# Kernel tuning notes

Hardware: AMD Instinct MI355X
Metric: run time of the kernel (lower is better)

Reference implementation:

```python
import jax, jax.numpy as jnp
import numpy as np

N_NODES = 50000
N_EDGES = 600000
N_GRAPHS = 512
HID = 128
LAT = 64
L = 4
BN_EPS = 1e-5


def _gelu(x):
    return jax.nn.gelu(x, approximate=False)


def _bn(x, g, b):
    m = jnp.mean(x, axis=0)
    v = jnp.var(x, axis=0)
    return (x - m) * jax.lax.rsqrt(v + BN_EPS) * g + b


def setup_inputs() -> dict:
    key = jax.random.key(0)
    ks = jax.random.split(key, 8)
    x = jax.random.normal(ks[0], (N_NODES, HID), dtype=jnp.float32)
    edge_index = jax.random.randint(ks[1], (2, N_EDGES), 0, N_NODES, dtype=jnp.int64 if jax.config.jax_enable_x64 else jnp.int32)
    batch = jnp.sort(jax.random.randint(ks[2], (N_NODES,), 0, N_GRAPHS))
    scale = 1.0 / np.sqrt(HID)
    return {
        "x": x,
        "edge_index": edge_index,
        "batch": batch,
        "input_bn_g": jnp.ones((HID,), jnp.float32),
        "input_bn_b": jnp.zeros((HID,), jnp.float32),
        "eps": jnp.zeros((L,), jnp.float32),
        "fc1_w": jax.random.normal(ks[3], (L, HID, HID), jnp.float32) * scale,
        "fc1_b": jnp.zeros((L, HID), jnp.float32),
        "bn1_g": jnp.ones((L, HID), jnp.float32),
        "bn1_b": jnp.zeros((L, HID), jnp.float32),
        "fc2_w": jax.random.normal(ks[4], (L, HID, HID), jnp.float32) * scale,
        "fc2_b": jnp.zeros((L, HID), jnp.float32),
        "bn_g": jnp.ones((L, HID), jnp.float32),
        "bn_b": jnp.zeros((L, HID), jnp.float32),
        "att_weight": jax.random.normal(ks[5], (L, HID), jnp.float32),
        "pool_weight": jnp.ones((3,), jnp.float32),
        "fcA_w": jax.random.normal(ks[6], (HID, HID), jnp.float32) * scale,
        "fcA_b": jnp.zeros((HID,), jnp.float32),
        "ln_g": jnp.ones((HID,), jnp.float32),
        "ln_b": jnp.zeros((HID,), jnp.float32),
        "fcB_w": jax.random.normal(ks[7], (HID, LAT), jnp.float32) * scale,
        "fcB_b": jnp.zeros((LAT,), jnp.float32),
    }


def reference(x, edge_index, batch, input_bn_g, input_bn_b, eps, fc1_w, fc1_b,
              bn1_g, bn1_b, fc2_w, fc2_b, bn_g, bn_b, att_weight, pool_weight,
              fcA_w, fcA_b, ln_g, ln_b, fcB_w, fcB_b):
    src, dst = edge_index[0], edge_index[1]
    x = _bn(x, input_bn_g, input_bn_b)  # input BatchNorm (batch stats)
    hidden_states = []
    for l in range(L):
        # GINConv: (1+eps)*x_i + sum_{j->i} x_j, then GatedResidualMLP
        agg = jax.ops.segment_sum(x[src], dst, num_segments=N_NODES)
        h = (1.0 + eps[l]) * x + agg
        h = _gelu(_bn(h @ fc1_w[l] + fc1_b[l], bn1_g[l], bn1_b[l]))
        h = h @ fc2_w[l] + fc2_b[l]
        h = _gelu(_bn(h, bn_g[l], bn_b[l]))
        hidden_states.append(h)
        x = h
    # JumpingKnowledge attention over layers
    x_all = jnp.stack(hidden_states, axis=0)               # [L, N, H]
    scores = jnp.mean(x_all * att_weight[:, None, :], -1)  # [L, N]
    alpha = jax.nn.softmax(scores, axis=0)
    x = jnp.sum(x_all * alpha[..., None], axis=0)          # [N, H]
    # fused add/mean/max pooling by graph id
    pw = jax.nn.softmax(pool_weight)
    sums = jax.ops.segment_sum(x, batch, num_segments=N_GRAPHS)
    cnt = jax.ops.segment_sum(jnp.ones((N_NODES, 1), x.dtype), batch, num_segments=N_GRAPHS)
    mean = sums / jnp.maximum(cnt, 1.0)
    mx = jax.ops.segment_max(x, batch, num_segments=N_GRAPHS)
    mx = jnp.where(cnt > 0, mx, 0.0)
    pooled = sums * pw[0] + mean * pw[1] + mx * pw[2]      # [G, H]
    out = pooled @ fcA_w + fcA_b
    mu = jnp.mean(out, -1, keepdims=True)
    var = jnp.var(out, -1, keepdims=True)
    out = (out - mu) * jax.lax.rsqrt(var + 1e-5) * ln_g + ln_b
    out = _gelu(out) + pooled
    return out @ fcB_w + fcB_b                              # [G, latent]
```

## Files before the change

kernel.cpp:

```cpp
#include <hip/hip_runtime.h>
#include <math.h>

#define N_NODES 50000
#define N_EDGES 600000
#define N_GRAPHS 512
#define HID 128
#define LAT 64
#define NL 4
#define SSTR 16
#define SSET 4096
#define N_TILES 3125
#define ZROWS 208
#define ZLD 136

typedef __attribute__((ext_vector_type(8))) __bf16 bf16x8;
typedef __attribute__((ext_vector_type(4))) float f32x4;

union Chunk {
    bf16x8 v;
    uint4 u4;
    ushort us[8];
};

__device__ __forceinline__ float gelu_exact(float x) {
    return 0.5f * x * (1.0f + erff(x * 0.70710678118654752f));
}
__device__ __forceinline__ float gelu_fast(float x) {
    float ax = fabsf(x) * 0.70710678118654752f;
    float t = __builtin_amdgcn_rcpf(fmaf(0.3275911f, ax, 1.0f));
    float p = t * (0.254829592f +
              t * (-0.284496736f +
              t * (1.421413741f +
              t * (-1.453152027f + t * 1.061405429f))));
    float e = __expf(-ax * ax);
    float erfv = 1.0f - p * e;
    float erfs = copysignf(erfv, x);
    return 0.5f * x * (1.0f + erfs);
}
__device__ __forceinline__ float bf2f(ushort h) {
    return __uint_as_float(((unsigned int)h) << 16);
}
__device__ __forceinline__ ushort f2bf(float f) {
    unsigned int u = __float_as_uint(f);
    unsigned int r = (u + 0x7FFFu + ((u >> 16) & 1u)) >> 16;
    return (ushort)r;
}
__device__ __forceinline__ void atomicMaxF(float* addr, float v) {
    if (v >= 0.f) atomicMax((int*)addr, __float_as_int(v));
    else atomicMin((unsigned int*)addr, __float_as_uint(v));
}

__device__ __forceinline__ void sub_range(int p, int j, int& s0, int& s1) {
    int r0 = (p * N_NODES) >> 8;
    int r1 = ((p + 1) * N_NODES) >> 8;
    int len = r1 - r0;
    s0 = r0 + ((len * j) >> 3);
    s1 = r0 + ((len * (j + 1)) >> 3);
}

template <bool NEWBAR>
__device__ __forceinline__ void grid_sync(int* bar, int epoch) {
    __syncthreads();
    if (threadIdx.x == 0) {
        int target = 256 * epoch;
        int prev = __hip_atomic_fetch_add(bar, 1, __ATOMIC_RELAXED,
                                          __HIP_MEMORY_SCOPE_AGENT);
        if (NEWBAR) {
            if (prev == target - 1) {
                __hip_atomic_store(bar + 32, epoch, __ATOMIC_RELAXED,
                                   __HIP_MEMORY_SCOPE_AGENT);
            } else {
                while (__hip_atomic_load(bar + 32, __ATOMIC_RELAXED,
                                         __HIP_MEMORY_SCOPE_AGENT) < epoch)
                    __builtin_amdgcn_s_sleep(8);
            }
        } else {
            while (__hip_atomic_load(bar, __ATOMIC_RELAXED,
                                     __HIP_MEMORY_SCOPE_AGENT) < target)
                __builtin_amdgcn_s_sleep(2);
        }
    }
    __syncthreads();
    asm volatile("" ::: "memory");
}

__device__ __forceinline__ float coh_ld(const float* p) {
    return __hip_atomic_load((const float*)p, __ATOMIC_RELAXED, __HIP_MEMORY_SCOPE_AGENT);
}

__global__ __launch_bounds__(256) void setup(const float* __restrict__ fc1w,
                                             const float* __restrict__ fc2w,
                                             ushort* __restrict__ Wt,
                                             int* __restrict__ counts,
                                             float* __restrict__ statsAll,
                                             float* __restrict__ psum,
                                             float* __restrict__ pmax,
                                             int* __restrict__ gstart,
                                             int* __restrict__ gend,
                                             int* __restrict__ bar) {
    int i = blockIdx.x * 256 + threadIdx.x;
    {
        int g = i >> 14;
        int rem = i & 16383;
        int n = rem >> 7, k = rem & 127;
        const float* W = (g < 4) ? (fc1w + (long)g * HID * HID)
                                 : (fc2w + (long)(g - 4) * HID * HID);
        Wt[i] = f2bf(W[k * HID + n]);
    }
    if (i < N_NODES) counts[i] = 0;
    if (i < 9 * SSET) statsAll[i] = 0.f;
    if (i < N_GRAPHS * HID) { psum[i] = 0.f; pmax[i] = -INFINITY; }
    if (i < N_GRAPHS) { gstart[i] = 0; gend[i] = 0; }
    if (i < 64) bar[i] = 0;
}

__global__ __launch_bounds__(256) void stats_count(const float* __restrict__ X,
                                                   float* __restrict__ stats,
                                                   const int* __restrict__ dst,
                                                   int* __restrict__ counts,
                                                   const int* __restrict__ batch,
                                                   int* __restrict__ gstart,
                                                   int* __restrict__ gend) {
    __shared__ float sh[2048];
    int bx = blockIdx.x;
    int t = threadIdx.x;
    if (bx < 256) {
        int tx = t & 31, ty = t >> 5;
        float s[4] = {0, 0, 0, 0}, q[4] = {0, 0, 0, 0};
        const int nTiles = (N_NODES + 63) / 64;
        for (int tile = bx; tile < nTiles; tile += 256) {
            int r0 = tile * 64;
#pragma unroll
            for (int i = 0; i < 8; ++i) {
                int r = r0 + ty + 8 * i;
                int rc = min(r, N_NODES - 1);
                float4 v = *(const float4*)(X + (long)rc * HID + 4 * tx);
                float w = (r < N_NODES) ? 1.f : 0.f;
                float x0 = v.x * w, x1 = v.y * w, x2 = v.z * w, x3 = v.w * w;
                s[0] += x0; s[1] += x1; s[2] += x2; s[3] += x3;
                q[0] += x0 * v.x; q[1] += x1 * v.y; q[2] += x2 * v.z; q[3] += x3 * v.w;
            }
        }
#pragma unroll
        for (int c = 0; c < 4; ++c) {
            sh[ty * HID + 4 * tx + c] = s[c];
            sh[1024 + ty * HID + 4 * tx + c] = q[c];
        }
        __syncthreads();
        if (ty == 0) {
#pragma unroll
            for (int c = 0; c < 4; ++c) {
                float a = 0, b = 0;
#pragma unroll
                for (int j = 0; j < 8; ++j) {
                    a += sh[j * HID + 4 * tx + c];
                    b += sh[1024 + j * HID + 4 * tx + c];
                }
                atomicAdd(stats + (4 * tx + c) * SSTR, a);
                atomicAdd(stats + (HID + 4 * tx + c) * SSTR, b);
            }
        }
    } else if (bx < 2600) {
        int e = (bx - 256) * 256 + t;
        if (e < N_EDGES) atomicAdd(counts + dst[e], 1);
    } else {
        int n = (bx - 2600) * 256 + t;
        if (n < N_NODES) {
            int b = batch[n];
            if (n == 0 || batch[n - 1] != b) gstart[b] = n;
            if (n == N_NODES - 1 || batch[n + 1] != b) gend[b] = n + 1;
        }
    }
}

__global__ __launch_bounds__(256) void bn_scan(const float* __restrict__ X,
                                               ushort* __restrict__ Y,
                                               const float* __restrict__ stats,
                                               const float* __restrict__ g,
                                               const float* __restrict__ b,
                                               const int* __restrict__ counts,
                                               int* __restrict__ offs,
                                               int* __restrict__ bsum) {
    __shared__ float scL[HID], sfL[HID];
    __shared__ int shI[256];
    int t = threadIdx.x;
    if (t < HID) {
        const float invN = 1.0f / (float)N_NODES;
        float mean = stats[t * SSTR] * invN;
        float var = stats[(HID + t) * SSTR] * invN - mean * mean;
        float s = g[t] * rsqrtf(var + 1e-5f);
        scL[t] = s;
        sfL[t] = b[t] - mean * s;
    }
    __syncthreads();
    int c4 = (t & 31) * 4;
    float sc[4], sf[4];
#pragma unroll
    for (int j = 0; j < 4; ++j) { sc[j] = scL[c4 + j]; sf[j] = sfL[c4 + j]; }
    int s0, s1;
    sub_range(blockIdx.x & 255, blockIdx.x >> 8, s0, s1);
    int c0 = s0 * 32, c1 = s1 * 32;
    for (int i = c0 + t; i < c1; i += 256) {
        float4 v = ((const float4*)X)[i];
        ushort4 w;
        w.x = f2bf(v.x * sc[0] + sf[0]);
        w.y = f2bf(v.y * sc[1] + sf[1]);
        w.z = f2bf(v.z * sc[2] + sf[2]);
        w.w = f2bf(v.w * sc[3] + sf[3]);
        ((ushort4*)Y)[i] = w;
    }
    if (blockIdx.x < 196) {
        int i = blockIdx.x * 256 + t;
        int v = (i < N_NODES) ? counts[i] : 0;
        shI[t] = v;
        __syncthreads();
        for (int off = 1; off < 256; off <<= 1) {
            int a = (t >= off) ? shI[t - off] : 0;
            __syncthreads();
            shI[t] += a;
            __syncthreads();
        }
        if (i < N_NODES) offs[i] = shI[t] - v;
        if (t == 255) bsum[blockIdx.x] = shI[255];
    }
}

__global__ __launch_bounds__(256) void scan23(int* __restrict__ offs,
                                              const int* __restrict__ bsum,
                                              int* __restrict__ cursor) {
    __shared__ int sh[256];
    int t = threadIdx.x, bx = blockIdx.x;
    int v = (t < bx) ? bsum[t] : 0;
    sh[t] = v;
    __syncthreads();
    for (int off = 128; off > 0; off >>= 1) {
        if (t < off) sh[t] += sh[t + off];
        __syncthreads();
    }
    int pre = sh[0];
    int i = bx * 256 + t;
    if (i < N_NODES) {
        int o = offs[i] + pre;
        offs[i] = o;
        cursor[i] = o;
    }
}

__global__ __launch_bounds__(256) void csr_fill(const int* __restrict__ src,
                                                const int* __restrict__ dst,
                                                int* __restrict__ cursor,
                                                int* __restrict__ csr) {
    int e = blockIdx.x * blockDim.x + threadIdx.x;
    if (e >= N_EDGES) return;
    int pos = atomicAdd(cursor + dst[e], 1);
    csr[pos] = src[e];
}

__global__ __launch_bounds__(256) void gin_gather_bf(const ushort* __restrict__ Xbf,
                                                     ushort* __restrict__ Hp,
                                                     const int* __restrict__ offs,
                                                     const int* __restrict__ counts,
                                                     const int* __restrict__ csr,
                                                     const float* __restrict__ eps, int l) {
    int t = threadIdx.x;
    int tx = t & 31;
    int grp = t >> 5;
    int s0, s1;
    sub_range(blockIdx.x & 255, blockIdx.x >> 8, s0, s1);
    float ev = 1.0f + eps[l];
    for (int node = s0 + grp; node < s1; node += 8) {
        ushort4 sv = *(const ushort4*)(Xbf + (long)node * HID + 4 * tx);
        float a0 = bf2f(sv.x) * ev, a1 = bf2f(sv.y) * ev;
        float a2 = bf2f(sv.z) * ev, a3 = bf2f(sv.w) * ev;
        int o = offs[node];
        int d = counts[node];
        int k = 0;
        for (; k + 8 <= d; k += 8) {
            int si[8];
#pragma unroll
            for (int j = 0; j < 8; ++j) si[j] = csr[o + k + j];
            ushort4 v[8];
#pragma unroll
            for (int j = 0; j < 8; ++j)
                v[j] = *(const ushort4*)(Xbf + (long)si[j] * HID + 4 * tx);
#pragma unroll
            for (int j = 0; j < 8; ++j) {
                a0 += bf2f(v[j].x); a1 += bf2f(v[j].y);
                a2 += bf2f(v[j].z); a3 += bf2f(v[j].w);
            }
        }
        for (; k + 4 <= d; k += 4) {
            int si[4];
#pragma unroll
            for (int j = 0; j < 4; ++j) si[j] = csr[o + k + j];
#pragma unroll
            for (int j = 0; j < 4; ++j) {
                ushort4 v = *(const ushort4*)(Xbf + (long)si[j] * HID + 4 * tx);
                a0 += bf2f(v.x); a1 += bf2f(v.y); a2 += bf2f(v.z); a3 += bf2f(v.w);
            }
        }
        for (; k < d; ++k) {
            int s = csr[o + k];
            ushort4 v = *(const ushort4*)(Xbf + (long)s * HID + 4 * tx);
            a0 += bf2f(v.x); a1 += bf2f(v.y); a2 += bf2f(v.z); a3 += bf2f(v.w);
        }
        ushort4 w;
        w.x = f2bf(a0); w.y = f2bf(a1); w.z = f2bf(a2); w.w = f2bf(a3);
        *(ushort4*)(Hp + (long)node * HID + 4 * tx) = w;
    }
}

template <int NT, bool NEWBAR>
__global__ __launch_bounds__(NT, 1) void fused_mlp(
    const ushort* __restrict__ Abf, const ushort* __restrict__ W1t,
    const ushort* __restrict__ W2t, const float* __restrict__ b1v,
    const float* __restrict__ b2v, const float* __restrict__ bn1g,
    const float* __restrict__ bn1b, const float* __restrict__ bn2g,
    const float* __restrict__ bn2b, float* __restrict__ st1,
    float* __restrict__ st2, ushort* __restrict__ Hl, int* __restrict__ bar,
    int epoch0) {
    constexpr int NW = NT / 64;
    constexpr int RSTEP = NW / 2;
    __shared__ __align__(16) ushort Z1[ZROWS * ZLD];
    __shared__ __align__(16) ushort Z2[ZROWS * ZLD];
    __shared__ float shs[2 * NT];
    __shared__ float scL[HID], sfL[HID];

    int t = threadIdx.x;
    int w = t >> 6, lane = t & 63;
    int m = lane & 15, q = lane >> 4;
    int c2 = w & 1, r2 = w >> 1;
    int t0 = (blockIdx.x * N_TILES) >> 8;
    int t1 = ((blockIdx.x + 1) * N_TILES) >> 8;

    bf16x8 Bf[4][4];
    {
        const ushort* Wh = W1t + (long)(c2 * 64) * HID;
#pragma unroll
        for (int nt = 0; nt < 4; ++nt)
#pragma unroll
            for (int kc = 0; kc < 4; ++kc)
                Bf[nt][kc] = *(const bf16x8*)(Wh + (nt * 16 + m) * HID + kc * 32 + q * 8);
    }
    float bias4[4];
#pragma unroll
    for (int nt = 0; nt < 4; ++nt) bias4[nt] = b1v[c2 * 64 + nt * 16 + m];

    float s_c[4] = {0, 0, 0, 0}, q_c[4] = {0, 0, 0, 0};
    int tile = t0 + r2;
    Chunk Ac[4];
    if (tile < t1) {
        const ushort* ar = Abf + (long)(tile * 16 + m) * HID + q * 8;
#pragma unroll
        for (int kc = 0; kc < 4; ++kc) Ac[kc].u4 = *(const uint4*)(ar + kc * 32);
    }
    while (tile < t1) {
        int nxt = tile + RSTEP;
        Chunk An[4];
        if (nxt < t1) {
            const ushort* ar = Abf + (long)(nxt * 16 + m) * HID + q * 8;
#pragma unroll
            for (int kc = 0; kc < 4; ++kc) An[kc].u4 = *(const uint4*)(ar + kc * 32);
        }
        f32x4 acc[4];
#pragma unroll
        for (int nt = 0; nt < 4; ++nt) acc[nt] = (f32x4){0.f, 0.f, 0.f, 0.f};
#pragma unroll
        for (int kc = 0; kc < 4; ++kc)
#pragma unroll
            for (int nt = 0; nt < 4; ++nt)
                acc[nt] = __builtin_amdgcn_mfma_f32_16x16x32_bf16(Ac[kc].v, Bf[nt][kc],
                                                                  acc[nt], 0, 0, 0);
        int lrow = (tile - t0) * 16;
#pragma unroll
        for (int nt = 0; nt < 4; ++nt) {
            int col = c2 * 64 + nt * 16 + m;
#pragma unroll
            for (int r = 0; r < 4; ++r) {
                float z = acc[nt][r] + bias4[nt];
                Z1[(lrow + q * 4 + r) * ZLD + col] = f2bf(z);
                s_c[nt] += z;
                q_c[nt] += z * z;
            }
        }
        tile = nxt;
#pragma unroll
        for (int kc = 0; kc < 4; ++kc) Ac[kc] = An[kc];
    }
#pragma unroll
    for (int nt = 0; nt < 4; ++nt) {
        s_c[nt] += __shfl_xor(s_c[nt], 16);
        s_c[nt] += __shfl_xor(s_c[nt], 32);
        q_c[nt] += __shfl_xor(q_c[nt], 16);
        q_c[nt] += __shfl_xor(q_c[nt], 32);
    }
    if (q == 0) {
#pragma unroll
        for (int nt = 0; nt < 4; ++nt) {
            shs[w * 64 + nt * 16 + m] = s_c[nt];
            shs[NT + w * 64 + nt * 16 + m] = q_c[nt];
        }
    }
    __syncthreads();
    if (t < HID) {
        int half = t >> 6, lc = t & 63;
        float a = 0.f, b = 0.f;
#pragma unroll
        for (int j = 0; j < RSTEP; ++j) {
            a += shs[(half + 2 * j) * 64 + lc];
            b += shs[NT + (half + 2 * j) * 64 + lc];
        }
        atomicAdd(st1 + t * SSTR, a);
        atomicAdd(st1 + (HID + t) * SSTR, b);
    }
    grid_sync<NEWBAR>(bar, epoch0 + 1);

    if (t < HID) {
        const float invN = 1.0f / (float)N_NODES;
        float mean = coh_ld(st1 + t * SSTR) * invN;
        float var = coh_ld(st1 + (HID + t) * SSTR) * invN - mean * mean;
        float s = bn1g[t] * rsqrtf(var + 1e-5f);
        scL[t] = s;
        sfL[t] = bn1b[t] - mean * s;
    }
    __syncthreads();

    {
        const ushort* Wh = W2t + (long)(c2 * 64) * HID;
#pragma unroll
        for (int nt = 0; nt < 4; ++nt)
#pragma unroll
            for (int kc = 0; kc < 4; ++kc)
                Bf[nt][kc] = *(const bf16x8*)(Wh + (nt * 16 + m) * HID + kc * 32 + q * 8);
    }
#pragma unroll
    for (int nt = 0; nt < 4; ++nt) bias4[nt] = b2v[c2 * 64 + nt * 16 + m];
#pragma unroll
    for (int nt = 0; nt < 4; ++nt) { s_c[nt] = 0.f; q_c[nt] = 0.f; }

    for (int tl = t0 + r2; tl < t1; tl += RSTEP) {
        int lrow = (tl - t0) * 16;
        Chunk Ax[4];
#pragma unroll
        for (int kc = 0; kc < 4; ++kc)
            Ax[kc].u4 = *(const uint4*)(Z1 + (lrow + m) * ZLD + kc * 32 + q * 8);
#pragma unroll
        for (int kc = 0; kc < 4; ++kc)
#pragma unroll
            for (int j = 0; j < 8; ++j) {
                int k = kc * 32 + q * 8 + j;
                float f = bf2f(Ax[kc].us[j]) * scL[k] + sfL[k];
                Ax[kc].us[j] = f2bf(gelu_fast(f));
            }
        f32x4 acc[4];
#pragma unroll
        for (int nt = 0; nt < 4; ++nt) acc[nt] = (f32x4){0.f, 0.f, 0.f, 0.f};
#pragma unroll
        for (int kc = 0; kc < 4; ++kc)
#pragma unroll
            for (int nt = 0; nt < 4; ++nt)
                acc[nt] = __builtin_amdgcn_mfma_f32_16x16x32_bf16(Ax[kc].v, Bf[nt][kc],
                                                                  acc[nt], 0, 0, 0);
#pragma unroll
        for (int nt = 0; nt < 4; ++nt) {
            int col = c2 * 64 + nt * 16 + m;
#pragma unroll
            for (int r = 0; r < 4; ++r) {
                float z = acc[nt][r] + bias4[nt];
                Z2[(lrow + q * 4 + r) * ZLD + col] = f2bf(z);
                s_c[nt] += z;
                q_c[nt] += z * z;
            }
        }
    }
#pragma unroll
    for (int nt = 0; nt < 4; ++nt) {
        s_c[nt] += __shfl_xor(s_c[nt], 16);
        s_c[nt] += __shfl_xor(s_c[nt], 32);
        q_c[nt] += __shfl_xor(q_c[nt], 16);
        q_c[nt] += __shfl_xor(q_c[nt], 32);
    }
    if (q == 0) {
#pragma unroll
        for (int nt = 0; nt < 4; ++nt) {
            shs[w * 64 + nt * 16 + m] = s_c[nt];
            shs[NT + w * 64 + nt * 16 + m] = q_c[nt];
        }
    }
    __syncthreads();
    if (t < HID) {
        int half = t >> 6, lc = t & 63;
        float a = 0.f, b = 0.f;
#pragma unroll
        for (int j = 0; j < RSTEP; ++j) {
            a += shs[(half + 2 * j) * 64 + lc];
            b += shs[NT + (half + 2 * j) * 64 + lc];
        }
        atomicAdd(st2 + t * SSTR, a);
        atomicAdd(st2 + (HID + t) * SSTR, b);
    }
    grid_sync<NEWBAR>(bar, epoch0 + 2);

    if (t < HID) {
        const float invN = 1.0f / (float)N_NODES;
        float mean = coh_ld(st2 + t * SSTR) * invN;
        float var = coh_ld(st2 + (HID + t) * SSTR) * invN - mean * mean;
        float s = bn2g[t] * rsqrtf(var + 1e-5f);
        scL[t] = s;
        sfL[t] = bn2b[t] - mean * s;
    }
    __syncthreads();

    int nch = (t1 - t0) * 16 * 16;
    for (int i = t; i < nch; i += NT) {
        int row = i >> 4, off = i & 15;
        Chunk ch;
        ch.u4 = *(const uint4*)(Z2 + row * ZLD + off * 8);
#pragma unroll
        for (int j = 0; j < 8; ++j) {
            int cc = off * 8 + j;
            float f = bf2f(ch.us[j]) * scL[cc] + sfL[cc];
            ch.us[j] = f2bf(gelu_fast(f));
        }
        *(uint4*)(Hl + (long)(t0 * 16 + row) * HID + off * 8) = ch.u4;
    }
}

__global__ __launch_bounds__(256) void jk_pool(const ushort* __restrict__ H0,
                                               const ushort* __restrict__ H1,
                                               const ushort* __restrict__ H2,
                                               const ushort* __restrict__ H3,
                                               const float* __restrict__ att,
                                               const int* __restrict__ batch,
                                               float* __restrict__ psum,
                                               float* __restrict__ pmax) {
    int t = threadIdx.x;
    int lane = t & 63, w = t >> 6;
    long wid = (long)blockIdx.x * 4 + w;
    int a0 = (int)((wid * N_NODES) >> 13);
    int a1 = (int)(((wid + 1) * N_NODES) >> 13);
    const ushort* Hs[4] = {H0, H1, H2, H3};
    float2 av[4];
#pragma unroll
    for (int l = 0; l < 4; ++l) av[l] = *(const float2*)(att + l * HID + 2 * lane);

    int curg = -1;
    float sx = 0.f, sy = 0.f, mx = -INFINITY, my = -INFINITY;
    for (int node = a0; node < a1; ++node) {
        int g = batch[node];
        if (g != curg) {
            if (curg >= 0) {
                float* ps = psum + (long)curg * HID + 2 * lane;
                float* pm = pmax + (long)curg * HID + 2 * lane;
                atomicAdd(ps, sx);
                atomicAdd(ps + 1, sy);
                atomicMaxF(pm, mx);
                atomicMaxF(pm + 1, my);
            }
            curg = g;
            sx = 0.f; sy = 0.f; mx = -INFINITY; my = -INFINITY;
        }
        float hx[4], hy[4], scr[4];
#pragma unroll
        for (int l = 0; l < 4; ++l) {
            unsigned int u = *(const unsigned int*)(Hs[l] + (long)node * HID + 2 * lane);
            float vx = bf2f((ushort)(u & 0xFFFF));
            float vy = bf2f((ushort)(u >> 16));
            hx[l] = vx; hy[l] = vy;
            float p = vx * av[l].x + vy * av[l].y;
#pragma unroll
            for (int off = 32; off > 0; off >>= 1) p += __shfl_xor(p, off);
            scr[l] = p * (1.0f / HID);
        }
        float mm = fmaxf(fmaxf(scr[0], scr[1]), fmaxf(scr[2], scr[3]));
        float e[4], se = 0.f;
#pragma unroll
        for (int l = 0; l < 4; ++l) { e[l] = expf(scr[l] - mm); se += e[l]; }
        float inv = 1.0f / se;
        float ox = 0.f, oy = 0.f;
#pragma unroll
        for (int l = 0; l < 4; ++l) {
            float a = e[l] * inv;
            ox += a * hx[l];
            oy += a * hy[l];
        }
        sx += ox; sy += oy;
        mx = fmaxf(mx, ox); my = fmaxf(my, oy);
    }
    if (curg >= 0) {
        float* ps = psum + (long)curg * HID + 2 * lane;
        float* pm = pmax + (long)curg * HID + 2 * lane;
        atomicAdd(ps, sx);
        atomicAdd(ps + 1, sy);
        atomicMaxF(pm, mx);
        atomicMaxF(pm + 1, my);
    }
}

__global__ __launch_bounds__(128) void finalize_head(const float* __restrict__ psum,
                                                     const float* __restrict__ pmax,
                                                     const int* __restrict__ gstart,
                                                     const int* __restrict__ gend,
                                                     const float* __restrict__ pw,
                                                     const float* __restrict__ fcAw,
                                                     const float* __restrict__ fcAb,
                                                     const float* __restrict__ lng,
                                                     const float* __restrict__ lnb,
                                                     const float* __restrict__ fcBw,
                                                     const float* __restrict__ fcBb,
                                                     float* __restrict__ out) {
    __shared__ float p[HID], qv[HID], red[HID];
    int g = blockIdx.x, j = threadIdx.x;
    float w0 = pw[0], w1 = pw[1], w2 = pw[2];
    float mw = fmaxf(w0, fmaxf(w1, w2));
    float e0 = expf(w0 - mw), e1 = expf(w1 - mw), e2 = expf(w2 - mw);
    float inv = 1.0f / (e0 + e1 + e2);
    e0 *= inv; e1 *= inv; e2 *= inv;
    int cnt = gend[g] - gstart[g];
    float s = psum[g * HID + j];
    float mx = pmax[g * HID + j];
    float mean0 = cnt > 0 ? s / (float)cnt : 0.f;
    float mxv = cnt > 0 ? mx : 0.f;
    float pool = s * e0 + mean0 * e1 + mxv * e2;
    p[j] = pool;
    __syncthreads();
    float acc = fcAb[j];
    for (int k = 0; k < HID; ++k) acc += p[k] * fcAw[k * HID + j];
    red[j] = acc;
    __syncthreads();
    for (int off = 64; off > 0; off >>= 1) {
        if (j < off) red[j] += red[j + off];
        __syncthreads();
    }
    float mean = red[0] * (1.0f / HID);
    __syncthreads();
    float d = acc - mean;
    red[j] = d * d;
    __syncthreads();
    for (int off = 64; off > 0; off >>= 1) {
        if (j < off) red[j] += red[j + off];
        __syncthreads();
    }
    float var = red[0] * (1.0f / HID);
    float y = d * rsqrtf(var + 1e-5f) * lng[j] + lnb[j];
    qv[j] = gelu_exact(y) + pool;
    __syncthreads();
    if (j < LAT) {
        float o = fcBb[j];
        for (int k = 0; k < HID; ++k) o += qv[k] * fcBw[k * LAT + j];
        out[g * LAT + j] = o;
    }
}

extern "C" void kernel_launch(void* const* d_in, const int* in_sizes, int n_in,
                              void* d_out, int out_size, void* d_ws, size_t ws_size,
                              hipStream_t stream) {
    const float* x = (const float*)d_in[0];
    const int* ei = (const int*)d_in[1];
    const int* src = ei;
    const int* dst = ei + N_EDGES;
    const int* batch = (const int*)d_in[2];
    const float* ibn_g = (const float*)d_in[3];
    const float* ibn_b = (const float*)d_in[4];
    const float* eps = (const float*)d_in[5];
    const float* fc1w = (const float*)d_in[6];
    const float* fc1b = (const float*)d_in[7];
    const float* bn1g = (const float*)d_in[8];
    const float* bn1b = (const float*)d_in[9];
    const float* fc2w = (const float*)d_in[10];
    const float* fc2b = (const float*)d_in[11];
    const float* bng = (const float*)d_in[12];
    const float* bnb = (const float*)d_in[13];
    const float* att = (const float*)d_in[14];
    const float* pw = (const float*)d_in[15];
    const float* fcAw = (const float*)d_in[16];
    const float* fcAb = (const float*)d_in[17];
    const float* lng = (const float*)d_in[18];
    const float* lnb = (const float*)d_in[19];
    const float* fcBw = (const float*)d_in[20];
    const float* fcBb = (const float*)d_in[21];
    float* out = (float*)d_out;

    const size_t NH = (size_t)N_NODES * HID;
    char* w8 = (char*)d_ws;
    ushort* x0bf = (ushort*)w8;     w8 += NH * 2;
    ushort* hprebf = (ushort*)w8;   w8 += NH * 2;
    ushort* Hlbf[NL];
    for (int l = 0; l < NL; ++l) { Hlbf[l] = (ushort*)w8; w8 += NH * 2; }
    float* statsAll = (float*)w8;   w8 += (size_t)9 * SSET * 4;
    float* psum = (float*)w8;       w8 += (size_t)N_GRAPHS * HID * 4;
    float* pmax = (float*)w8;       w8 += (size_t)N_GRAPHS * HID * 4;
    int* gstart = (int*)w8;         w8 += N_GRAPHS * 4;
    int* gend = (int*)w8;           w8 += N_GRAPHS * 4;
    int* counts = (int*)w8;         w8 += N_NODES * 4;
    int* offs = (int*)w8;           w8 += N_NODES * 4;
    int* cursor = (int*)w8;         w8 += N_NODES * 4;
    int* bsum = (int*)w8;           w8 += 256 * 4;
    int* csr = (int*)w8;            w8 += (size_t)N_EDGES * 4;
    ushort* WtBf = (ushort*)w8;     w8 += (size_t)8 * HID * HID * 2;
    int* bar = (int*)w8;            w8 += 64 * 4;

    const int edgeBlocks = (N_EDGES + 255) / 256;

    setup<<<512, 256, 0, stream>>>(fc1w, fc2w, WtBf, counts, statsAll, psum, pmax,
                                   gstart, gend, bar);
    stats_count<<<256 + edgeBlocks + 196, 256, 0, stream>>>(x, statsAll, dst, counts,
                                                            batch, gstart, gend);
    bn_scan<<<2048, 256, 0, stream>>>(x, x0bf, statsAll, ibn_g, ibn_b, counts, offs,
                                      bsum);
    scan23<<<196, 256, 0, stream>>>(offs, bsum, cursor);
    csr_fill<<<edgeBlocks, 256, 0, stream>>>(src, dst, cursor, csr);

    const ushort* xin = x0bf;
    for (int l = 0; l < NL; ++l) {
        float* st1 = statsAll + (size_t)(1 + 2 * l) * SSET;
        float* st2 = statsAll + (size_t)(2 + 2 * l) * SSET;
        gin_gather_bf<<<2048, 256, 0, stream>>>(xin, hprebf, offs, counts, csr, eps, l);
        if (l == 0 || l == 2) {
            fused_mlp<512, true><<<256, 512, 0, stream>>>(
                hprebf, WtBf + (size_t)l * HID * HID,
                WtBf + (size_t)(4 + l) * HID * HID, fc1b + l * HID, fc2b + l * HID,
                bn1g + l * HID, bn1b + l * HID, bng + l * HID, bnb + l * HID,
                st1, st2, Hlbf[l], bar, 2 * l);
        } else {
            fused_mlp<512, false><<<256, 512, 0, stream>>>(
                hprebf, WtBf + (size_t)l * HID * HID,
                WtBf + (size_t)(4 + l) * HID * HID, fc1b + l * HID, fc2b + l * HID,
                bn1g + l * HID, bn1b + l * HID, bng + l * HID, bnb + l * HID,
                st1, st2, Hlbf[l], bar, 2 * l);
        }
        xin = Hlbf[l];
    }

    jk_pool<<<2048, 256, 0, stream>>>(Hlbf[0], Hlbf[1], Hlbf[2], Hlbf[3], att, batch,
                                      psum, pmax);
    finalize_head<<<N_GRAPHS, 128, 0, stream>>>(psum, pmax, gstart, gend, pw, fcAw,
                                                fcAb, lng, lnb, fcBw, fcBb, out);
}
```

Measured before the change: 491.3 us.

## Use hierarchical grid barrier and group-partitioned BN stats atomics

Replaces the flat grid barrier in layers 0 and 2 with a two-level barrier. Blocks arrive on one of 16 group counters, and the last arrival in each group bumps a master counter that releases a flag. BatchNorm sum and sum-of-squares atomics from the input stats pass and the fused MLP are spread across 16 partial copies, which readers then reduce, to cut same-address atomic contention. Layers 1 and 3 move to the flag-based single-counter barrier. In exchange, setup must zero a partial-stats buffer of several MB, and every reader does 16 coherent loads per channel.

```diff
diff --git a/kernel.cpp b/kernel.cpp
--- a/kernel.cpp
+++ b/kernel.cpp
@@ -9,6 +9,8 @@
 #define NL 4
 #define SSTR 16
 #define SSET 4096
+#define NGRP 16
+#define PSET (NGRP * 256 * SSTR)
 #define N_TILES 3125
 #define ZROWS 208
 #define ZLD 136
@@ -58,15 +60,28 @@
     s1 = r0 + ((len * (j + 1)) >> 3);
 }
 
-template <bool NEWBAR>
+template <bool GROUPED>
 __device__ __forceinline__ void grid_sync(int* bar, int epoch) {
     __syncthreads();
     if (threadIdx.x == 0) {
-        int target = 256 * epoch;
-        int prev = __hip_atomic_fetch_add(bar, 1, __ATOMIC_RELAXED,
-                                          __HIP_MEMORY_SCOPE_AGENT);
-        if (NEWBAR) {
-            if (prev == target - 1) {
+        if (GROUPED) {
+            int g = blockIdx.x & (NGRP - 1);
+            int prev = __hip_atomic_fetch_add(bar + 64 + g * 16, 1, __ATOMIC_RELAXED,
+                                              __HIP_MEMORY_SCOPE_AGENT);
+            if (prev == NGRP * epoch - 1) {
+                int mp = __hip_atomic_fetch_add(bar + 320, 1, __ATOMIC_RELAXED,
+                                                __HIP_MEMORY_SCOPE_AGENT);
+                if (mp == NGRP * epoch - 1)
+                    __hip_atomic_store(bar + 336, epoch, __ATOMIC_RELAXED,
+                                       __HIP_MEMORY_SCOPE_AGENT);
+            }
+            while (__hip_atomic_load(bar + 336, __ATOMIC_RELAXED,
+                                     __HIP_MEMORY_SCOPE_AGENT) < epoch)
+                __builtin_amdgcn_s_sleep(4);
+        } else {
+            int prev = __hip_atomic_fetch_add(bar, 1, __ATOMIC_RELAXED,
+                                              __HIP_MEMORY_SCOPE_AGENT);
+            if (prev == 256 * epoch - 1) {
                 __hip_atomic_store(bar + 32, epoch, __ATOMIC_RELAXED,
                                    __HIP_MEMORY_SCOPE_AGENT);
             } else {
@@ -74,10 +89,6 @@
                                          __HIP_MEMORY_SCOPE_AGENT) < epoch)
                     __builtin_amdgcn_s_sleep(8);
             }
-        } else {
-            while (__hip_atomic_load(bar, __ATOMIC_RELAXED,
-                                     __HIP_MEMORY_SCOPE_AGENT) < target)
-                __builtin_amdgcn_s_sleep(2);
         }
     }
     __syncthreads();
@@ -93,6 +104,7 @@
                                              ushort* __restrict__ Wt,
                                              int* __restrict__ counts,
                                              float* __restrict__ statsAll,
+                                             float* __restrict__ statsPart,
                                              float* __restrict__ psum,
                                              float* __restrict__ pmax,
                                              int* __restrict__ gstart,
@@ -109,13 +121,14 @@
     }
     if (i < N_NODES) counts[i] = 0;
     if (i < 9 * SSET) statsAll[i] = 0.f;
+    for (long j = i; j < (long)9 * PSET; j += 131072) statsPart[j] = 0.f;
     if (i < N_GRAPHS * HID) { psum[i] = 0.f; pmax[i] = -INFINITY; }
     if (i < N_GRAPHS) { gstart[i] = 0; gend[i] = 0; }
-    if (i < 64) bar[i] = 0;
+    if (i < 512) bar[i] = 0;
 }
 
 __global__ __launch_bounds__(256) void stats_count(const float* __restrict__ X,
-                                                   float* __restrict__ stats,
+                                                   float* __restrict__ inPart,
                                                    const int* __restrict__ dst,
                                                    int* __restrict__ counts,
                                                    const int* __restrict__ batch,
@@ -148,6 +161,8 @@
         }
         __syncthreads();
         if (ty == 0) {
+            int grp = bx & (NGRP - 1);
+            float* base = inPart + (long)(grp * 256) * SSTR;
 #pragma unroll
             for (int c = 0; c < 4; ++c) {
                 float a = 0, b = 0;
@@ -156,8 +171,8 @@
                     a += sh[j * HID + 4 * tx + c];
                     b += sh[1024 + j * HID + 4 * tx + c];
                 }
-                atomicAdd(stats + (4 * tx + c) * SSTR, a);
-                atomicAdd(stats + (HID + 4 * tx + c) * SSTR, b);
+                atomicAdd(base + (4 * tx + c) * SSTR, a);
+                atomicAdd(base + (HID + 4 * tx + c) * SSTR, b);
             }
         }
     } else if (bx < 2600) {
@@ -175,7 +190,7 @@
 
 __global__ __launch_bounds__(256) void bn_scan(const float* __restrict__ X,
                                                ushort* __restrict__ Y,
-                                               const float* __restrict__ stats,
+                                               const float* __restrict__ inPart,
                                                const float* __restrict__ g,
                                                const float* __restrict__ b,
                                                const int* __restrict__ counts,
@@ -185,9 +200,15 @@
     __shared__ int shI[256];
     int t = threadIdx.x;
     if (t < HID) {
+        float sm = 0.f, sq = 0.f;
+#pragma unroll
+        for (int gg = 0; gg < NGRP; ++gg) {
+            sm += inPart[((long)gg * 256 + t) * SSTR];
+            sq += inPart[((long)gg * 256 + HID + t) * SSTR];
+        }
         const float invN = 1.0f / (float)N_NODES;
-        float mean = stats[t * SSTR] * invN;
-        float var = stats[(HID + t) * SSTR] * invN - mean * mean;
+        float mean = sm * invN;
+        float var = sq * invN - mean * mean;
         float s = g[t] * rsqrtf(var + 1e-5f);
         scL[t] = s;
         sfL[t] = b[t] - mean * s;
@@ -310,7 +331,7 @@
     }
 }
 
-template <int NT, bool NEWBAR>
+template <int NT, bool GROUPED>
 __global__ __launch_bounds__(NT, 1) void fused_mlp(
     const ushort* __restrict__ Abf, const ushort* __restrict__ W1t,
     const ushort* __restrict__ W2t, const float* __restrict__ b1v,
@@ -332,6 +353,7 @@
     int c2 = w & 1, r2 = w >> 1;
     int t0 = (blockIdx.x * N_TILES) >> 8;
     int t1 = ((blockIdx.x + 1) * N_TILES) >> 8;
+    int grp = blockIdx.x & (NGRP - 1);
 
     bf16x8 Bf[4][4];
     {
@@ -410,15 +432,33 @@
             a += shs[(half + 2 * j) * 64 + lc];
             b += shs[NT + (half + 2 * j) * 64 + lc];
         }
-        atomicAdd(st1 + t * SSTR, a);
-        atomicAdd(st1 + (HID + t) * SSTR, b);
-    }
-    grid_sync<NEWBAR>(bar, epoch0 + 1);
+        if (GROUPED) {
+            float* base = st1 + (long)(grp * 256) * SSTR;
+            atomicAdd(base + t * SSTR, a);
+            atomicAdd(base + (HID + t) * SSTR, b);
+        } else {
+            atomicAdd(st1 + t * SSTR, a);
+            atomicAdd(st1 + (HID + t) * SSTR, b);
+        }
+    }
+    grid_sync<GROUPED>(bar, epoch0 + 1);
 
     if (t < HID) {
+        float sm, sq;
+        if (GROUPED) {
+            sm = 0.f; sq = 0.f;
+#pragma unroll
+            for (int gg = 0; gg < NGRP; ++gg) {
+                sm += coh_ld(st1 + ((long)gg * 256 + t) * SSTR);
+                sq += coh_ld(st1 + ((long)gg * 256 + HID + t) * SSTR);
+            }
+        } else {
+            sm = coh_ld(st1 + t * SSTR);
+            sq = coh_ld(st1 + (HID + t) * SSTR);
+        }
         const float invN = 1.0f / (float)N_NODES;
-        float mean = coh_ld(st1 + t * SSTR) * invN;
-        float var = coh_ld(st1 + (HID + t) * SSTR) * invN - mean * mean;
+        float mean = sm * invN;
+        float var = sq * invN - mean * mean;
         float s = bn1g[t] * rsqrtf(var + 1e-5f);
         scL[t] = s;
         sfL[t] = bn1b[t] - mean * s;
@@ -496,15 +536,33 @@
             a += shs[(half + 2 * j) * 64 + lc];
             b += shs[NT + (half + 2 * j) * 64 + lc];
         }
-        atomicAdd(st2 + t * SSTR, a);
-        atomicAdd(st2 + (HID + t) * SSTR, b);
-    }
-    grid_sync<NEWBAR>(bar, epoch0 + 2);
+        if (GROUPED) {
+            float* base = st2 + (long)(grp * 256) * SSTR;
+            atomicAdd(base + t * SSTR, a);
+            atomicAdd(base + (HID + t) * SSTR, b);
+        } else {
+            atomicAdd(st2 + t * SSTR, a);
+            atomicAdd(st2 + (HID + t) * SSTR, b);
+        }
+    }
+    grid_sync<GROUPED>(bar, epoch0 + 2);
 
     if (t < HID) {
+        float sm, sq;
+        if (GROUPED) {
+            sm = 0.f; sq = 0.f;
+#pragma unroll
+            for (int gg = 0; gg < NGRP; ++gg) {
+                sm += coh_ld(st2 + ((long)gg * 256 + t) * SSTR);
+                sq += coh_ld(st2 + ((long)gg * 256 + HID + t) * SSTR);
+            }
+        } else {
+            sm = coh_ld(st2 + t * SSTR);
+            sq = coh_ld(st2 + (HID + t) * SSTR);
+        }
         const float invN = 1.0f / (float)N_NODES;
-        float mean = coh_ld(st2 + t * SSTR) * invN;
-        float var = coh_ld(st2 + (HID + t) * SSTR) * invN - mean * mean;
+        float mean = sm * invN;
+        float var = sq * invN - mean * mean;
         float s = bn2g[t] * rsqrtf(var + 1e-5f);
         scL[t] = s;
         sfL[t] = bn2b[t] - mean * s;
@@ -688,6 +746,7 @@
     ushort* Hlbf[NL];
     for (int l = 0; l < NL; ++l) { Hlbf[l] = (ushort*)w8; w8 += NH * 2; }
     float* statsAll = (float*)w8;   w8 += (size_t)9 * SSET * 4;
+    float* statsPart = (float*)w8;  w8 += (size_t)9 * PSET * 4;
     float* psum = (float*)w8;       w8 += (size_t)N_GRAPHS * HID * 4;
     float* pmax = (float*)w8;       w8 += (size_t)N_GRAPHS * HID * 4;
     int* gstart = (int*)w8;         w8 += N_GRAPHS * 4;
@@ -698,36 +757,38 @@
     int* bsum = (int*)w8;           w8 += 256 * 4;
     int* csr = (int*)w8;            w8 += (size_t)N_EDGES * 4;
     ushort* WtBf = (ushort*)w8;     w8 += (size_t)8 * HID * HID * 2;
-    int* bar = (int*)w8;            w8 += 64 * 4;
+    int* bar = (int*)w8;            w8 += 512 * 4;
 
     const int edgeBlocks = (N_EDGES + 255) / 256;
 
-    setup<<<512, 256, 0, stream>>>(fc1w, fc2w, WtBf, counts, statsAll, psum, pmax,
-                                   gstart, gend, bar);
-    stats_count<<<256 + edgeBlocks + 196, 256, 0, stream>>>(x, statsAll, dst, counts,
+    setup<<<512, 256, 0, stream>>>(fc1w, fc2w, WtBf, counts, statsAll, statsPart,
+                                   psum, pmax, gstart, gend, bar);
+    stats_count<<<256 + edgeBlocks + 196, 256, 0, stream>>>(x, statsPart, dst, counts,
                                                             batch, gstart, gend);
-    bn_scan<<<2048, 256, 0, stream>>>(x, x0bf, statsAll, ibn_g, ibn_b, counts, offs,
+    bn_scan<<<2048, 256, 0, stream>>>(x, x0bf, statsPart, ibn_g, ibn_b, counts, offs,
                                       bsum);
     scan23<<<196, 256, 0, stream>>>(offs, bsum, cursor);
     csr_fill<<<edgeBlocks, 256, 0, stream>>>(src, dst, cursor, csr);
 
     const ushort* xin = x0bf;
     for (int l = 0; l < NL; ++l) {
-        float* st1 = statsAll + (size_t)(1 + 2 * l) * SSET;
-        float* st2 = statsAll + (size_t)(2 + 2 * l) * SSET;
         gin_gather_bf<<<2048, 256, 0, stream>>>(xin, hprebf, offs, counts, csr, eps, l);
         if (l == 0 || l == 2) {
+            float* p1 = statsPart + (size_t)(1 + 2 * l) * PSET;
+            float* p2 = statsPart + (size_t)(2 + 2 * l) * PSET;
             fused_mlp<512, true><<<256, 512, 0, stream>>>(
                 hprebf, WtBf + (size_t)l * HID * HID,
                 WtBf + (size_t)(4 + l) * HID * HID, fc1b + l * HID, fc2b + l * HID,
                 bn1g + l * HID, bn1b + l * HID, bng + l * HID, bnb + l * HID,
-                st1, st2, Hlbf[l], bar, 2 * l);
+                p1, p2, Hlbf[l], bar, (l == 0) ? 0 : 2);
         } else {
+            float* st1 = statsAll + (size_t)(1 + 2 * l) * SSET;
+            float* st2 = statsAll + (size_t)(2 + 2 * l) * SSET;
             fused_mlp<512, false><<<256, 512, 0, stream>>>(
                 hprebf, WtBf + (size_t)l * HID * HID,
                 WtBf + (size_t)(4 + l) * HID * HID, fc1b + l * HID, fc2b + l * HID,
                 bn1g + l * HID, bn1b + l * HID, bng + l * HID, bnb + l * HID,
-                st1, st2, Hlbf[l], bar, 2 * l);
+                st1, st2, Hlbf[l], bar, (l == 1) ? 0 : 2);
         }
         xin = Hlbf[l];
     }
```

Measured after the change: 490.3 us. No clear change (-0.2%).
